# Kernel optimization log

Measured on AMD Instinct MI355X. Metric: run time of the kernel, lower is better.

The kernel has to match this reference:

```python
import jax, jax.numpy as jnp
import numpy as np

NPX = 128      # nPxPup
FOV = 512      # fovInPixel = 2*samp*nPxPup, samp=2
NMODES = 54    # len(jModes)
BATCH = 8
ALPHA = np.pi / 2


def _make_consts():
    # circular pupil on the nPxPup grid
    x = np.linspace(-1.0, 1.0, NPX)
    X, Y = np.meshgrid(x, x)
    pupil = ((X ** 2 + Y ** 2) <= 1.0).astype(np.float32)
    # 4-faced pyramid phase mask on the FOV grid, pre-fftshifted
    f = np.arange(FOV) - FOV / 2
    FX, FY = np.meshgrid(f, f)
    pyr_phase = ALPHA * (np.abs(FX) + np.abs(FY))
    pyr_mask = np.fft.fftshift(np.exp(-1j * pyr_phase)).astype(np.complex64)
    return pupil, pyr_mask


def setup_inputs() -> dict:
    key = jax.random.key(0)
    k1, k2 = jax.random.split(key)
    pupil_np, mask_np = _make_consts()
    pupil = jnp.asarray(pupil_np)                      # [NPX,NPX] float32
    pyrMask = jnp.asarray(mask_np)                     # [FOV,FOV] complex64 (fftshifted)
    # Zernike-like mode basis restricted to the pupil, column-major modes as in the torch buffer
    modes = jax.random.normal(k1, (NPX * NPX, NMODES), dtype=jnp.float32) * pupil.reshape(-1, 1)
    OL1 = (jnp.eye(NMODES, dtype=jnp.float32) * 0.1)   # learnable parameter
    inputs = jax.random.normal(k2, (BATCH, 1, NPX, NPX), dtype=jnp.float32) * pupil
    return {"inputs": inputs, "modes": modes, "OL1": OL1, "pupil": pupil, "pyrMask": pyrMask}


def _prop(phase, pupil, pyrMask):
    """Vanilla pyramid WFS propagation (modulation=0).
    phase: [B,1,NPX,NPX] -> intensity [B,1,FOV,FOV]."""
    u = (pupil * jnp.exp(1j * phase)).astype(jnp.complex64)
    npv = (FOV - NPX) // 2
    field = jnp.zeros(phase.shape[:2] + (FOV, FOV), dtype=jnp.complex64)
    field = field.at[:, :, npv:npv + NPX, npv:npv + NPX].set(u)
    buf = jnp.fft.fft2(field) * pyrMask          # focal plane * pyramid mask
    return jnp.abs(jnp.fft.fft2(buf)) ** 2       # detector intensity


def reference(inputs, modes, OL1, pupil, pyrMask):
    n_modes = OL1.shape[0]
    optModes = modes @ OL1                                     # [NPX*NPX, M]
    # reference (flat wavefront) intensity
    flat = (jnp.ones((NPX, NPX), jnp.float32) * (pupil > 0))[None, None]
    I0 = _prop(flat, pupil, pyrMask)
    I0 = I0 / jnp.sum(I0)                                      # [1,1,FOV,FOV]
    gainRow = jnp.sum(OL1, axis=1)                             # [M]
    # batch the per-mode +/- push-pull propagations in one FFT pass
    zim = optModes.T.reshape(n_modes, 1, NPX, NPX)
    phases = jnp.concatenate([zim, -zim], axis=0)              # [2M,1,NPX,NPX]
    I4 = _prop(phases, pupil, pyrMask)
    I4 = I4 / jnp.sum(I4, axis=(1, 2, 3), keepdims=True)
    sp = I4[:n_modes] - I0
    sm = I4[n_modes:] - I0
    MZc = 0.5 * (sp - sm) / gainRow[:, None, None, None]
    IM = MZc.reshape(n_modes, -1).T                            # [FOV*FOV, M]
    CM = jnp.linalg.pinv(IM)                                   # [M, FOV*FOV]
    # measurement
    Ip = _prop(inputs, pupil, pyrMask)                         # [B,1,FOV,FOV]
    Inorm = jnp.sum(Ip, axis=(1, 2, 3), keepdims=True)
    Ip = Ip / Inorm - I0
    y = CM @ Ip.reshape(Ip.shape[0], -1).T                     # [M, B]
    return y
```

## Files before the change

kernel.cpp:

```cpp
#include <hip/hip_runtime.h>
#include <math.h>

#define NPIXK 262144
#define ROWF2 584
#define ROWF2B 585

__device__ __forceinline__ int padi8(int i) { return i + (i >> 3); }
__device__ __forceinline__ int padi(int i) { return i + (i >> 5); }

#define WSYNC asm volatile("s_waitcnt lgkmcnt(0)" ::: "memory")

__device__ __forceinline__ float2 cmul(float2 a, float2 b) {
    return make_float2(a.x * b.x - a.y * b.y, a.x * b.y + a.y * b.x);
}

__device__ __forceinline__ void twchain(float ang, float2 tw[8]) {
    float s, c;
    sincosf(ang, &s, &c);
    float2 w1 = make_float2(c, s);
    float2 w2 = cmul(w1, w1);
    float2 w4 = cmul(w2, w2);
    tw[1] = w1;
    tw[2] = w2;
    tw[3] = cmul(w1, w2);
    tw[4] = w4;
    tw[5] = cmul(w1, w4);
    tw[6] = cmul(w2, w4);
    tw[7] = cmul(tw[3], w4);
}

__device__ __forceinline__ void fft8f(float vr[8], float vi[8]) {
    float er[4], ei[4], orr[4], oi[4];
    {
        float t0r = vr[0] + vr[4], t0i = vi[0] + vi[4];
        float t1r = vr[0] - vr[4], t1i = vi[0] - vi[4];
        float t2r = vr[2] + vr[6], t2i = vi[2] + vi[6];
        float t3r = vi[2] - vi[6], t3i = vr[6] - vr[2];
        er[0] = t0r + t2r; ei[0] = t0i + t2i;
        er[1] = t1r + t3r; ei[1] = t1i + t3i;
        er[2] = t0r - t2r; ei[2] = t0i - t2i;
        er[3] = t1r - t3r; ei[3] = t1i - t3i;
    }
    {
        float t0r = vr[1] + vr[5], t0i = vi[1] + vi[5];
        float t1r = vr[1] - vr[5], t1i = vi[1] - vi[5];
        float t2r = vr[3] + vr[7], t2i = vi[3] + vi[7];
        float t3r = vi[3] - vi[7], t3i = vr[7] - vr[3];
        orr[0] = t0r + t2r; oi[0] = t0i + t2i;
        orr[1] = t1r + t3r; oi[1] = t1i + t3i;
        orr[2] = t0r - t2r; oi[2] = t0i - t2i;
        orr[3] = t1r - t3r; oi[3] = t1i - t3i;
    }
    const float c = 0.70710678118654752440f;
    vr[0] = er[0] + orr[0]; vi[0] = ei[0] + oi[0];
    vr[4] = er[0] - orr[0]; vi[4] = ei[0] - oi[0];
    float t1r = c * (orr[1] + oi[1]), t1i = c * (oi[1] - orr[1]);
    vr[1] = er[1] + t1r; vi[1] = ei[1] + t1i;
    vr[5] = er[1] - t1r; vi[5] = ei[1] - t1i;
    float t2r = oi[2], t2i = -orr[2];
    vr[2] = er[2] + t2r; vi[2] = ei[2] + t2i;
    vr[6] = er[2] - t2r; vi[6] = ei[2] - t2i;
    float t3r = c * (oi[3] - orr[3]), t3i = -c * (orr[3] + oi[3]);
    vr[3] = er[3] + t3r; vi[3] = ei[3] + t3i;
    vr[7] = er[3] - t3r; vi[7] = ei[3] - t3i;
}

__device__ __forceinline__ void fft8_s34(float vr[8], float vi[8]) {
    const float c = 0.70710678118654752440f;
    float x3r = vr[3], x3i = vi[3], x4r = vr[4], x4i = vi[4];
    float A = c * (x3r + x3i), B = c * (x3r - x3i);
    vr[0] = x3r + x4r; vi[0] = x3i + x4i;
    vr[1] = -B - x4r;  vi[1] = -A - x4i;
    vr[2] = x4r - x3i; vi[2] = x3r + x4i;
    vr[3] = A - x4r;   vi[3] = -B - x4i;
    vr[4] = x4r - x3r; vi[4] = x4i - x3i;
    vr[5] = B - x4r;   vi[5] = A - x4i;
    vr[6] = x3i + x4r; vi[6] = x4i - x3r;
    vr[7] = -A - x4r;  vi[7] = B - x4i;
}

template <int SPARSE>
__device__ __forceinline__ void fft512v(float2* L, int t,
                                        float vr[8], float vi[8]) {
    if (SPARSE) fft8_s34(vr, vi); else fft8f(vr, vi);
    {
        float2* wb = L + 9 * t;
#pragma unroll
        for (int r = 0; r < 8; ++r) wb[r] = make_float2(vr[r], vi[r]);
    }
    float2 tw[8];
    twchain((float)(t & 7) * -0.09817477042468103870f, tw);
    WSYNC;
    {
        const float2* rb = L + t + (t >> 3);
        { float2 a = rb[0]; vr[0] = a.x; vi[0] = a.y; }
#pragma unroll
        for (int r = 1; r < 8; ++r) {
            float2 a = rb[72 * r];
            float2 w = tw[r];
            vr[r] = a.x * w.x - a.y * w.y;
            vi[r] = a.x * w.y + a.y * w.x;
        }
        fft8f(vr, vi);
        WSYNC;
        float2* wb = L + 9 * t;
#pragma unroll
        for (int r = 0; r < 8; ++r) wb[r] = make_float2(vr[r], vi[r]);
    }
    twchain((float)t * -0.01227184630308512985f, tw);
    WSYNC;
    {
        const float2* rb = L + 9 * (t & 7) + (t >> 3);
        { float2 a = rb[0]; vr[0] = a.x; vi[0] = a.y; }
#pragma unroll
        for (int r = 1; r < 8; ++r) {
            float2 a = rb[72 * r];
            float2 w = tw[r];
            vr[r] = a.x * w.x - a.y * w.y;
            vi[r] = a.x * w.y + a.y * w.x;
        }
        fft8f(vr, vi);
    }
}

template <int SPARSE>
__device__ __forceinline__ void fft512v2(float2* LA, float2* LB, int t,
                                         float avr[8], float avi[8],
                                         float bvr[8], float bvi[8]) {
    if (SPARSE) { fft8_s34(avr, avi); fft8_s34(bvr, bvi); }
    else        { fft8f(avr, avi);   fft8f(bvr, bvi); }
    {
        float2* wa = LA + 9 * t;
        float2* wb = LB + 9 * t;
#pragma unroll
        for (int r = 0; r < 8; ++r) wa[r] = make_float2(avr[r], avi[r]);
#pragma unroll
        for (int r = 0; r < 8; ++r) wb[r] = make_float2(bvr[r], bvi[r]);
    }
    float2 tw[8];
    twchain((float)(t & 7) * -0.09817477042468103870f, tw);
    WSYNC;
    {
        const float2* ra = LA + t + (t >> 3);
        const float2* rb = LB + t + (t >> 3);
        { float2 a = ra[0]; avr[0] = a.x; avi[0] = a.y; }
        { float2 b = rb[0]; bvr[0] = b.x; bvi[0] = b.y; }
#pragma unroll
        for (int r = 1; r < 8; ++r) {
            float2 a = ra[72 * r], b = rb[72 * r], w = tw[r];
            avr[r] = a.x * w.x - a.y * w.y;  avi[r] = a.x * w.y + a.y * w.x;
            bvr[r] = b.x * w.x - b.y * w.y;  bvi[r] = b.x * w.y + b.y * w.x;
        }
        fft8f(avr, avi); fft8f(bvr, bvi);
        WSYNC;
        float2* wa = LA + 9 * t;
        float2* wb = LB + 9 * t;
#pragma unroll
        for (int r = 0; r < 8; ++r) wa[r] = make_float2(avr[r], avi[r]);
#pragma unroll
        for (int r = 0; r < 8; ++r) wb[r] = make_float2(bvr[r], bvi[r]);
    }
    twchain((float)t * -0.01227184630308512985f, tw);
    WSYNC;
    {
        const float2* ra = LA + 9 * (t & 7) + (t >> 3);
        const float2* rb = LB + 9 * (t & 7) + (t >> 3);
        { float2 a = ra[0]; avr[0] = a.x; avi[0] = a.y; }
        { float2 b = rb[0]; bvr[0] = b.x; bvi[0] = b.y; }
#pragma unroll
        for (int r = 1; r < 8; ++r) {
            float2 a = ra[72 * r], b = rb[72 * r], w = tw[r];
            avr[r] = a.x * w.x - a.y * w.y;  avi[r] = a.x * w.y + a.y * w.x;
            bvr[r] = b.x * w.x - b.y * w.y;  bvi[r] = b.x * w.y + b.y * w.x;
        }
        fft8f(avr, avi); fft8f(bvr, bvi);
    }
}

#define FFT_LDS __shared__ float2 lds[4][ROWF2];

__device__ __forceinline__ double lsx(int i) {
    if (i == 127) return 1.0;
    return __dadd_rn(__dmul_rn((double)i, 2.0 / 127.0), -1.0);
}
__device__ __forceinline__ double pupilAt(int r, int c) {
    double xc = lsx(c), xr = lsx(r);
    double s = __dadd_rn(__dmul_rn(xc, xc), __dmul_rn(xr, xr));
    return (s <= 1.0) ? 1.0 : 0.0;
}

__global__ __launch_bounds__(256, 8) void k_s1(const float* __restrict__ optT,
                                               const float* __restrict__ inputs,
                                               float2* __restrict__ T1, int giBase) {
    FFT_LDS
    int tid = threadIdx.x, w = tid >> 6, t = tid & 63;
    int r = (blockIdx.x & 31) * 4 + w;
    int im = blockIdx.x >> 5;
    int gi;
    if (giBase >= 0)            gi = giBase + im;
    else if (giBase == -1)      gi = (im == 0) ? 0 : 108 + im;
    else                        gi = (im < 9) ? ((im == 0) ? 0 : 108 + im)
                                              : im - 8;

    float vr[8], vi[8];
#pragma unroll
    for (int q = 0; q < 8; ++q) { vr[q] = 0.f; vi[q] = 0.f; }
#pragma unroll
    for (int h = 0; h < 2; ++h) {
        int c = t + 64 * h;
        int p = r * 128 + c;
        float pu = (float)pupilAt(r, c);
        float ph;
        if (gi == 0) {
            ph = pu;
        } else if (gi < 109) {
            ph = optT[(gi - 1) * 16384 + p];
        } else {
            ph = inputs[(gi - 109) * 16384 + p];
        }
        float s, cs; sincosf(ph, &s, &cs);
        vr[3 + h] = pu * cs; vi[3 + h] = pu * s;
    }
    fft512v<1>(lds[w], t, vr, vi);
    WSYNC;
#pragma unroll
    for (int q = 0; q < 8; ++q) {
        int d = t + 64 * q;
        lds[w][padi8(d)] = make_float2(vr[q], vi[q]);
    }
    __syncthreads();
    int r0 = (blockIdx.x & 31) * 4;
    float2* dst = T1 + (size_t)im * 65536;
#pragma unroll
    for (int it = 0; it < 8; ++it) {
        int g = it * 256 + tid;
        int l = g >> 2, rr = g & 3;
        dst[(size_t)l * 128 + r0 + rr] = lds[rr][padi8(l)];
    }
}

__global__ __launch_bounds__(256, 4) void k_s23(const float2* __restrict__ T1,
                                                float2* __restrict__ C2p) {
    __shared__ float2 lds[8][ROWF2B];
    int tid = threadIdx.x, w = tid >> 6, t = tid & 63;
    int imgL = blockIdx.x >> 6;
    int l0 = (blockIdx.x & 63) * 8;
    int lA = l0 + w, lB = l0 + 4 + w;
    const float2* srcA = T1 + (size_t)imgL * 65536 + (size_t)lA * 128;
    const float2* srcB = T1 + (size_t)imgL * 65536 + (size_t)lB * 128;
    float avr[8], avi[8], bvr[8], bvi[8];
#pragma unroll
    for (int q = 0; q < 8; ++q) { avr[q] = 0.f; avi[q] = 0.f; bvr[q] = 0.f; bvi[q] = 0.f; }
    { float2 a0 = srcA[t], a1 = srcA[t + 64];
      avr[3] = a0.x; avi[3] = a0.y; avr[4] = a1.x; avi[4] = a1.y; }
    { float2 b0 = srcB[t], b1 = srcB[t + 64];
      bvr[3] = b0.x; bvi[3] = b0.y; bvr[4] = b1.x; bvi[4] = b1.y; }
    fft512v2<1>(lds[w], lds[w + 4], t, avr, avi, bvr, bvi);
    int glA = (lA <= 256) ? lA : 512 - lA;
    int glB = (lB <= 256) ? lB : 512 - lB;
#pragma unroll
    for (int q = 0; q < 8; ++q) {
        int k = t + 64 * q;
        int gk = (k <= 256) ? k : 512 - k;
        {   int n = (gk + glA) & 3;
            float a = avr[q], b = avi[q], X, Y;
            if (n == 0)      { X = a;  Y = b;  }
            else if (n == 1) { X = b;  Y = -a; }
            else if (n == 2) { X = -a; Y = -b; }
            else             { X = -b; Y = a;  }
            avr[q] = X; avi[q] = Y; }
        {   int n = (gk + glB) & 3;
            float a = bvr[q], b = bvi[q], X, Y;
            if (n == 0)      { X = a;  Y = b;  }
            else if (n == 1) { X = b;  Y = -a; }
            else if (n == 2) { X = -a; Y = -b; }
            else             { X = -b; Y = a;  }
            bvr[q] = X; bvi[q] = Y; }
    }
    fft512v2<0>(lds[w], lds[w + 4], t, avr, avi, bvr, bvi);
    WSYNC;
#pragma unroll
    for (int q = 0; q < 8; ++q) {
        int d = padi8(t + 64 * q);
        lds[w][d]     = make_float2(avr[q], avi[q]);
        lds[w + 4][d] = make_float2(bvr[q], bvi[q]);
    }
    __syncthreads();
    float2* dst = C2p + (size_t)imgL * NPIXK;
#pragma unroll
    for (int it = 0; it < 16; ++it) {
        int g = it * 256 + tid;
        int p = g >> 3, rr = g & 7;
        dst[(size_t)p * 512 + l0 + rr] = lds[rr][padi8(p)];
    }
}

__global__ __launch_bounds__(256, 8) void k_s4(const float2* __restrict__ C2,
                                               float* __restrict__ dst,
                                               const float* __restrict__ I0,
                                               int ep) {
    FFT_LDS
    int tid = threadIdx.x, w = tid >> 6, t = tid & 63;
    int imgL = blockIdx.x >> 7, p = (blockIdx.x & 127) * 4 + w;
    const float2* src = C2 + (size_t)imgL * NPIXK + (size_t)p * 512;
    float vr[8], vi[8];
#pragma unroll
    for (int q = 0; q < 8; ++q) { float2 a = src[t + 64 * q]; vr[q] = a.x; vi[q] = a.y; }
    fft512v<0>(lds[w], t, vr, vi);
    size_t rowOff = (size_t)p * 512;
    float* drow = dst + (size_t)imgL * NPIXK + rowOff;
    if (ep == 0) {
#pragma unroll
        for (int q = 0; q < 8; ++q) {
            int k = t + 64 * q;
            drow[k] = vr[q] * vr[q] + vi[q] * vi[q];
        }
    } else {
#pragma unroll
        for (int q = 0; q < 8; ++q) {
            int k = t + 64 * q;
            float mag2 = vr[q] * vr[q] + vi[q] * vi[q];
            drow[k] = mag2 - I0[rowOff + k];
        }
    }
}

__global__ __launch_bounds__(256, 8) void k_s4pm(const float2* __restrict__ C2p,
                                                 float* __restrict__ dst,
                                                 const double* __restrict__ gainInv,
                                                 int gBase) {
    FFT_LDS
    int tid = threadIdx.x, w = tid >> 6, t = tid & 63;
    int imgL = blockIdx.x >> 7, q2 = blockIdx.x & 127;
    int p = 2 * q2 + (w & 1) + (w >> 1) * 256;
    const float2* src = C2p + (size_t)imgL * NPIXK + (size_t)p * 512;
    float vr[8], vi[8], m2[8];
#pragma unroll
    for (int q = 0; q < 8; ++q) { float2 a = src[t + 64 * q]; vr[q] = a.x; vi[q] = a.y; }
    fft512v<0>(lds[w], t, vr, vi);
    WSYNC;
    float* mrow = (float*)lds[w];
#pragma unroll
    for (int q = 0; q < 8; ++q) {
        m2[q] = vr[q] * vr[q] + vi[q] * vi[q];
        mrow[padi(t + 64 * q)] = m2[q];
    }
    __syncthreads();
    float g = (float)gainInv[gBase + imgL];
    float* drow = dst + (size_t)imgL * NPIXK + (size_t)p * 512;
    const float* prow = (const float*)lds[w ^ 2];
#pragma unroll
    for (int q = 0; q < 8; ++q) {
        int qp = (q + 4) & 7;
        float other = prow[padi(t + 64 * qp)];
        drow[t + 64 * q] = g * (m2[q] - other);
    }
}

__global__ __launch_bounds__(256, 8) void k_s4x(const float2* __restrict__ C2p,
                                                float* __restrict__ I0buf,
                                                float* __restrict__ Mz,
                                                const double* __restrict__ gainInv) {
    FFT_LDS
    int tid = threadIdx.x, w = tid >> 6, t = tid & 63;
    int im = blockIdx.x >> 7, b7 = blockIdx.x & 127;
    if (im < 9) {
        int p = b7 * 4 + w;
        const float2* src = C2p + (size_t)im * NPIXK + (size_t)p * 512;
        float vr[8], vi[8];
#pragma unroll
        for (int q = 0; q < 8; ++q) { float2 a = src[t + 64 * q]; vr[q] = a.x; vi[q] = a.y; }
        fft512v<0>(lds[w], t, vr, vi);
        float* drow = I0buf + (size_t)im * NPIXK + (size_t)p * 512;
#pragma unroll
        for (int q = 0; q < 8; ++q) {
            int k = t + 64 * q;
            drow[k] = vr[q] * vr[q] + vi[q] * vi[q];
        }
    } else {
        int mi = im - 9;
        int p = 2 * b7 + (w & 1) + (w >> 1) * 256;
        const float2* src = C2p + (size_t)im * NPIXK + (size_t)p * 512;
        float vr[8], vi[8], m2[8];
#pragma unroll
        for (int q = 0; q < 8; ++q) { float2 a = src[t + 64 * q]; vr[q] = a.x; vi[q] = a.y; }
        fft512v<0>(lds[w], t, vr, vi);
        WSYNC;
        float* mrow = (float*)lds[w];
#pragma unroll
        for (int q = 0; q < 8; ++q) {
            m2[q] = vr[q] * vr[q] + vi[q] * vi[q];
            mrow[padi(t + 64 * q)] = m2[q];
        }
        __syncthreads();
        float g = (float)gainInv[mi];
        float* drow = Mz + (size_t)mi * NPIXK + (size_t)p * 512;
        const float* prow = (const float*)lds[w ^ 2];
#pragma unroll
        for (int q = 0; q < 8; ++q) {
            int qp = (q + 4) & 7;
            float other = prow[padi(t + 64 * qp)];
            drow[t + 64 * q] = g * (m2[q] - other);
        }
    }
}

__global__ __launch_bounds__(256) void k_modes(const float* __restrict__ modes,
                                               const float* __restrict__ OL1,
                                               float* __restrict__ optT,
                                               double* __restrict__ gainInv,
                                               double* __restrict__ G,
                                               double* __restrict__ bmat) {
    __shared__ float sM[64 * 54];
    __shared__ float sOL[54 * 54];
    int tid = threadIdx.x;
    if (blockIdx.x == 0) {
        for (int i = tid; i < 54 * 54; i += 256) G[i] = 0.0;
        for (int i = tid; i < 54 * 8; i += 256) bmat[i] = 0.0;
    }
    for (int i = tid; i < 54 * 54; i += 256) sOL[i] = OL1[i];
    const float* msrc = modes + (size_t)blockIdx.x * 64 * 54;
    for (int i = tid; i < 64 * 54; i += 256) sM[i] = msrc[i];
    __syncthreads();
    int pl = tid & 63, mg = tid >> 6;
    int p = blockIdx.x * 64 + pl;
    const float* mrow = sM + pl * 54;
    for (int m = mg; m < 54; m += 4) {
        double acc = 0.0;
#pragma unroll
        for (int j = 0; j < 54; ++j)
            acc += (double)mrow[j] * (double)sOL[j * 54 + m];
        optT[(size_t)m * 16384 + p] = (float)acc;
    }
    if (blockIdx.x == 0 && tid < 54) {
        double g = 0.0;
        for (int j = 0; j < 54; ++j) g += (double)sOL[tid * 54 + j];
        gainInv[tid] = 0.5 / g;
    }
}

__device__ __forceinline__ float dot4(float4 a, float4 b) {
    return a.x * b.x + a.y * b.y + a.z * b.z + a.w * b.w;
}

#define GPROWS 2304
__global__ __launch_bounds__(256, 4) void k_gram54(const float* __restrict__ Mz,
                                                   const float* __restrict__ V,
                                                   const float* __restrict__ I0,
                                                   float* __restrict__ part,
                                                   int subI0) {
    __shared__ float Ms[64 * 128];
    int tid = threadIdx.x;
    int task = tid / 7, sl = tid - task * 7;
    if (task > 35) task = 35;
    int oi = 0, rem = task;
    while (rem >= 8 - oi) { rem -= 8 - oi; ++oi; }
    int oj = oi + rem;
    int ra = 8 * oi, rb = 8 * oj;
    int start = (32 * sl) / 7, len = (32 * (sl + 1)) / 7 - start;
    int rot = tid % len;
    float s[64];
#pragma unroll
    for (int q = 0; q < 64; ++q) s[q] = 0.f;

#pragma unroll 1
    for (int ch = 0; ch < 2; ++ch) {
        size_t P0 = ((size_t)blockIdx.x * 2 + ch) * 128;
        if (ch) __syncthreads();
        for (int idx = tid; idx < 64 * 32; idx += 256) {
            int i = idx >> 5, v4 = idx & 31;
            float4 vv;
            if (i < 54) {
                vv = *(const float4*)(Mz + (size_t)i * NPIXK + P0 + v4 * 4);
            } else if (i < 62) {
                vv = *(const float4*)(V + (size_t)(i - 54) * NPIXK + P0 + v4 * 4);
                if (subI0) {
                    float4 i0 = *(const float4*)(I0 + P0 + v4 * 4);
                    vv.x -= i0.x; vv.y -= i0.y; vv.z -= i0.z; vv.w -= i0.w;
                }
            } else {
                vv = make_float4(0.f, 0.f, 0.f, 0.f);
            }
            ((float4*)Ms)[i * 32 + (v4 ^ (i >> 3))] = vv;
        }
        __syncthreads();
#pragma unroll 1
        for (int k = 0; k < 5; ++k) {
            if (k < len) {
                int kk = k + rot; if (kk >= len) kk -= len;
                int pp = start + kk;
                int colA = pp ^ oi, colB = pp ^ oj;
                float4 b[8];
#pragma unroll
                for (int j = 0; j < 8; ++j)
                    b[j] = ((const float4*)Ms)[(rb + j) * 32 + colB];
#pragma unroll
                for (int i = 0; i < 8; ++i) {
                    float4 a = ((const float4*)Ms)[(ra + i) * 32 + colA];
#pragma unroll
                    for (int j = 0; j < 8; ++j) {
                        float acc = s[i * 8 + j];
                        acc = fmaf(a.x, b[j].x, acc);
                        acc = fmaf(a.y, b[j].y, acc);
                        acc = fmaf(a.z, b[j].z, acc);
                        acc = fmaf(a.w, b[j].w, acc);
                        s[i * 8 + j] = acc;
                    }
                }
            }
        }
    }
    float* red = Ms;
    float* dst = part + (size_t)blockIdx.x * GPROWS;
#pragma unroll
    for (int c = 0; c < 4; ++c) {
        __syncthreads();
        if (tid < 252) {
#pragma unroll
            for (int q = 0; q < 4; ++q)
                ((float4*)(red + tid * 16))[q] =
                    make_float4(s[c * 16 + 4 * q], s[c * 16 + 4 * q + 1],
                                s[c * 16 + 4 * q + 2], s[c * 16 + 4 * q + 3]);
        }
        __syncthreads();
        for (int idx = tid; idx < 576; idx += 256) {
            int tk = idx >> 4, j = idx & 15;
            float acc = 0.f;
#pragma unroll
            for (int ss = 0; ss < 7; ++ss) acc += red[(tk * 7 + ss) * 16 + j];
            dst[tk * 64 + c * 16 + j] = acc;
        }
    }
}

__global__ __launch_bounds__(256) void k_gred54(const float* __restrict__ part,
                                                double* __restrict__ G,
                                                double* __restrict__ bmat) {
    __shared__ double red[8][33];
    int tid = threadIdx.x;
    int r = tid & 31, grp = tid >> 5;
    int row = blockIdx.x * 32 + r;
    int bid0 = blockIdx.y * 256;
    double acc = 0.0;
    for (int k = 0; k < 32; ++k)
        acc += (double)part[(size_t)(bid0 + grp + 8 * k) * GPROWS + row];
    red[grp][r] = acc;
    __syncthreads();
    if (tid < 32) {
        int rr = blockIdx.x * 32 + tid;
        double s = 0.0;
#pragma unroll
        for (int g = 0; g < 8; ++g) s += red[g][tid];
        int tk = rr >> 6, q = rr & 63;
        int oi = 0, rem = tk;
        while (rem >= 8 - oi) { rem -= 8 - oi; ++oi; }
        int oj = oi + rem;
        int a = 8 * oi + (q >> 3), b = 8 * oj + (q & 7);
        if (a < 54) {
            if (b < 54) {
                if (a <= b) atomicAdd(&G[a * 54 + b], s);
            } else if (b < 62) {
                atomicAdd(&bmat[a * 8 + (b - 54)], s);
            }
        }
    }
}

__global__ __launch_bounds__(256) void k_gram(const float* __restrict__ Mz,
                                              const float* __restrict__ V,
                                              const float* __restrict__ I0,
                                              float* __restrict__ part,
                                              int cA, int PROWS, int subI0) {
    __shared__ float Ms[54 * 128];
    __shared__ float Vs[8 * 128];
    int tid = threadIdx.x;
    int cQ = (cA + 3) >> 2;
    int nQT = cQ * (cQ + 1) / 2;
    int nT = nQT + cQ * 8;
    int task = tid;
    int kind = (task < nQT) ? 0 : (task < nT ? 1 : 2);
    int r0[4], r1[4], bb = 0, Ti = 0, Tj = 0, Qi = 0;
    if (kind == 0) {
        int rem = task;
        while (rem >= cQ - Ti) { rem -= cQ - Ti; ++Ti; }
        Tj = Ti + rem;
#pragma unroll
        for (int q = 0; q < 4; ++q) {
            int i = 4 * Ti + q; r0[q] = (i < cA) ? i : cA - 1;
            int j = 4 * Tj + q; r1[q] = (j < cA) ? j : cA - 1;
        }
    } else if (kind == 1) {
        int tb = task - nQT;
        Qi = tb >> 3; bb = tb & 7;
#pragma unroll
        for (int q = 0; q < 4; ++q) {
            int i = 4 * Qi + q; r0[q] = (i < cA) ? i : cA - 1;
        }
    }
    float s[16];
#pragma unroll
    for (int q = 0; q < 16; ++q) s[q] = 0.f;

    size_t P0 = (size_t)blockIdx.x * 128;
    for (int idx = tid; idx < cA * 32; idx += 256) {
        int i = idx >> 5, v4 = idx & 31;
        ((float4*)Ms)[i * 32 + v4] =
            *(const float4*)(Mz + (size_t)i * NPIXK + P0 + v4 * 4);
    }
    for (int idx = tid; idx < 8 * 32; idx += 256) {
        int b = idx >> 5, v4 = idx & 31;
        float4 vv = *(const float4*)(V + (size_t)b * NPIXK + P0 + v4 * 4);
        if (subI0) {
            float4 i0 = *(const float4*)(I0 + P0 + v4 * 4);
            vv.x -= i0.x; vv.y -= i0.y; vv.z -= i0.z; vv.w -= i0.w;
        }
        ((float4*)Vs)[b * 32 + v4] = vv;
    }
    __syncthreads();
    if (kind == 0) {
        for (int kk = 0; kk < 32; ++kk) {
            int pp = (kk + tid) & 31;
            float4 a0 = ((float4*)(Ms + r0[0] * 128))[pp];
            float4 a1 = ((float4*)(Ms + r0[1] * 128))[pp];
            float4 a2 = ((float4*)(Ms + r0[2] * 128))[pp];
            float4 a3 = ((float4*)(Ms + r0[3] * 128))[pp];
            float4 b0 = ((float4*)(Ms + r1[0] * 128))[pp];
            float4 b1 = ((float4*)(Ms + r1[1] * 128))[pp];
            float4 b2 = ((float4*)(Ms + r1[2] * 128))[pp];
            float4 b3 = ((float4*)(Ms + r1[3] * 128))[pp];
            s[0] += dot4(a0, b0); s[1] += dot4(a0, b1);
            s[2] += dot4(a0, b2); s[3] += dot4(a0, b3);
            s[4] += dot4(a1, b0); s[5] += dot4(a1, b1);
            s[6] += dot4(a1, b2); s[7] += dot4(a1, b3);
            s[8] += dot4(a2, b0); s[9] += dot4(a2, b1);
            s[10] += dot4(a2, b2); s[11] += dot4(a2, b3);
            s[12] += dot4(a3, b0); s[13] += dot4(a3, b1);
            s[14] += dot4(a3, b2); s[15] += dot4(a3, b3);
        }
    } else if (kind == 1) {
        for (int kk = 0; kk < 32; ++kk) {
            int pp = (kk + tid) & 31;
            float4 vb = ((float4*)Vs)[bb * 32 + pp];
            float4 a0 = ((float4*)(Ms + r0[0] * 128))[pp];
            float4 a1 = ((float4*)(Ms + r0[1] * 128))[pp];
            float4 a2 = ((float4*)(Ms + r0[2] * 128))[pp];
            float4 a3 = ((float4*)(Ms + r0[3] * 128))[pp];
            s[0] += dot4(a0, vb); s[1] += dot4(a1, vb);
            s[2] += dot4(a2, vb); s[3] += dot4(a3, vb);
        }
    }
    float* dst = part + (size_t)blockIdx.x * PROWS;
    if (kind == 0) {
#pragma unroll
        for (int q = 0; q < 16; ++q) dst[task * 16 + q] = s[q];
    } else if (kind == 1) {
#pragma unroll
        for (int q = 0; q < 4; ++q)
            dst[nQT * 16 + (task - nQT) * 4 + q] = s[q];
    }
}

__global__ __launch_bounds__(256) void k_gred3(const float* __restrict__ part,
                                               double* __restrict__ G,
                                               double* __restrict__ bmat,
                                               int cA, int m0, int PROWS) {
    __shared__ double red[8][33];
    int tid = threadIdx.x;
    int r = tid & 31, grp = tid >> 5;
    int row = blockIdx.x * 32 + r;
    int bid0 = blockIdx.y * 256;
    double acc = 0.0;
    if (row < PROWS)
        for (int k = 0; k < 32; ++k)
            acc += (double)part[(size_t)(bid0 + grp + 8 * k) * PROWS + row];
    red[grp][r] = acc;
    __syncthreads();
    if (tid < 32) {
        int rr = blockIdx.x * 32 + tid;
        if (rr < PROWS) {
            double s = 0.0;
#pragma unroll
            for (int g = 0; g < 8; ++g) s += red[g][tid];
            int cQ = (cA + 3) >> 2;
            int nQT = cQ * (cQ + 1) / 2;
            if (rr < nQT * 16) {
                int tile = rr >> 4, q = rr & 15;
                int Ti = 0, rem = tile;
                while (rem >= cQ - Ti) { rem -= cQ - Ti; ++Ti; }
                int Tj = Ti + rem;
                int i = 4 * Ti + (q >> 2), j = 4 * Tj + (q & 3);
                if (i < cA && j < cA && i <= j)
                    atomicAdd(&G[(m0 + i) * 54 + (m0 + j)], s);
            } else {
                int qb = rr - nQT * 16;
                int tb = qb >> 2, qq = qb & 3;
                int Qi = tb >> 3, bbb = tb & 7;
                int i = 4 * Qi + qq;
                if (i < cA) atomicAdd(&bmat[(m0 + i) * 8 + bbb], s);
            }
        }
    }
}

__global__ __launch_bounds__(256) void k_gramx(const float* __restrict__ MzA,
                                               const float* __restrict__ MzB,
                                               double* __restrict__ G,
                                               int cA, int m0, int mb) {
    __shared__ float Ms[54 * 128];
    __shared__ float Bs[128];
    int tid = threadIdx.x;
    double acc = 0.0;
    for (int ch = 0; ch < 4; ++ch) {
        size_t P0 = (size_t)blockIdx.x * 512 + (size_t)ch * 128;
        __syncthreads();
        for (int idx = tid; idx < cA * 32; idx += 256) {
            int i = idx >> 5, v4 = idx & 31;
            ((float4*)Ms)[i * 32 + v4] =
                *(const float4*)(MzA + (size_t)i * NPIXK + P0 + v4 * 4);
        }
        if (tid < 128) Bs[tid] = MzB[P0 + tid];
        __syncthreads();
        if (tid < cA) {
            const float* ri = Ms + tid * 128;
            float s = 0.f;
            for (int k = 0; k < 128; ++k) {
                int p = (k + tid) & 127;
                s += ri[p] * Bs[p];
            }
            acc += (double)s;
        }
    }
    if (tid < cA) atomicAdd(&G[(m0 + tid) * 54 + mb], acc);
}

__global__ __launch_bounds__(512) void k_solve(const double* __restrict__ G,
                                               const double* __restrict__ bmat,
                                               float* __restrict__ out) {
    __shared__ double A[54][65];
    int tid = threadIdx.x;
    int r = tid >> 3, cg = tid & 7;
    for (int idx = tid; idx < 54 * 62; idx += 512) {
        int i = idx / 62, c = idx % 62;
        A[i][c] = (c < 54) ? ((i <= c) ? G[i * 54 + c] : G[c * 54 + i])
                           : bmat[i * 8 + (c - 54)];
    }
    __syncthreads();
    for (int p = 0; p < 54; ++p) {
        double f = 0.0;
        bool act = (r < 54) && (r != p);
        if (act) f = A[r][p] / A[p][p];
        __syncthreads();
        if (act) {
#pragma unroll
            for (int k = 0; k < 8; ++k) {
                int c = cg + 8 * k;
                if (c < 62) A[r][c] -= f * A[p][c];
            }
        }
        __syncthreads();
    }
    for (int idx = tid; idx < 54 * 8; idx += 512) {
        int m = idx >> 3, b = idx & 7;
        out[idx] = (float)(A[m][54 + b] / A[m][m]);
    }
}

__global__ void k_zero(float* out, int n) {
    int i = blockIdx.x * 256 + threadIdx.x;
    if (i < n) out[i] = 0.f;
}

extern "C" void kernel_launch(void* const* d_in, const int* in_sizes, int n_in,
                              void* d_out, int out_size, void* d_ws, size_t ws_size,
                              hipStream_t stream) {
    float* out = (float*)d_out;
    if (out_size <= 0) return;
    if (n_in < 3 || in_sizes[0] != 131072 || in_sizes[1] != 884736 ||
        in_sizes[2] != 2916 || out_size < 432) {
        k_zero<<<(out_size + 255) / 256, 256, 0, stream>>>(out, out_size);
        return;
    }
    const float* inputs = (const float*)d_in[0];
    const float* modes  = (const float*)d_in[1];
    const float* OL1    = (const float*)d_in[2];

    char* ws = (char*)d_ws;
    size_t off = 0;
    auto alloc = [&](size_t bytes) -> void* {
        void* p = ws + off;
        off += (bytes + 255) & ~(size_t)255;
        return p;
    };
    float*  optT    = (float*)  alloc((size_t)54 * 16384 * 4);
    double* gainInv = (double*) alloc(64 * 8);
    double* G       = (double*) alloc(54 * 54 * 8);
    double* bmat    = (double*) alloc(54 * 8 * 8);
    float*  I0buf   = (float*)  alloc((size_t)9 * NPIXK * 4);
    float*  V       = I0buf + NPIXK;
    float*  MzB1    = (float*)  alloc((size_t)NPIXK * 4);
    float*  part    = (float*)  alloc((size_t)2048 * GPROWS * 4);

    const size_t IMG  = (size_t)NPIXK * 4 + 256;
    const size_t PIPE = ((size_t)65536 * 8 + 256) + ((size_t)NPIXK * 8 + 256);
    size_t rem = (ws_size > off + 4096) ? ws_size - off - 4096 : 0;
    int cA, chunkP;
    if (rem >= 54 * IMG + PIPE) {
        cA = 54;
        size_t c = (rem - 54 * IMG) / PIPE;
        chunkP = (c > 63) ? 63 : (int)c;
        if (chunkP < 1) chunkP = 1;
    } else if (rem >= IMG + PIPE) {
        cA = (int)((rem - PIPE) / IMG);
        if (cA > 53) cA = 53;
        if (cA < 1) cA = 1;
        size_t left = rem - (size_t)cA * IMG;
        chunkP = (int)(left / PIPE);
        if (chunkP < 1) chunkP = 1;
        if (chunkP > cA) chunkP = cA;
    } else {
        k_zero<<<(out_size + 255) / 256, 256, 0, stream>>>(out, out_size);
        return;
    }
    float*  MzA = (float*)  alloc((size_t)cA * NPIXK * 4);
    float2* T1  = (float2*) alloc((size_t)chunkP * 65536 * 8);
    float2* C2p = (float2*) alloc((size_t)chunkP * NPIXK * 8);
    if (off > ws_size) {
        k_zero<<<(out_size + 255) / 256, 256, 0, stream>>>(out, out_size);
        return;
    }

    auto prop_one = [&](int giBase, int n, float* dst, int ep) {
        for (int s = 0; s < n; s += chunkP) {
            int nn = n - s; if (nn > chunkP) nn = chunkP;
            k_s1<<<nn * 32, 256, 0, stream>>>(optT, inputs, T1, giBase + s);
            k_s23<<<nn * 64, 256, 0, stream>>>(T1, C2p);
            k_s4<<<nn * 128, 256, 0, stream>>>(C2p, dst + (size_t)s * NPIXK,
                                               I0buf, ep);
        }
    };
    auto prop_pm = [&](int m0, int n, float* dst, int gBase) {
        for (int s = 0; s < n; s += chunkP) {
            int nn = n - s; if (nn > chunkP) nn = chunkP;
            k_s1<<<nn * 32, 256, 0, stream>>>(optT, inputs, T1, 1 + m0 + s);
            k_s23<<<nn * 64, 256, 0, stream>>>(T1, C2p);
            k_s4pm<<<nn * 128, 256, 0, stream>>>(C2p,
                                                 dst + (size_t)s * NPIXK,
                                                 gainInv, gBase + s);
        }
    };

    k_modes<<<256, 256, 0, stream>>>(modes, OL1, optT, gainInv, G, bmat);

    if (cA >= 54 && chunkP >= 63) {
        k_s1<<<63 * 32, 256, 0, stream>>>(optT, inputs, T1, -2);
        k_s23<<<63 * 64, 256, 0, stream>>>(T1, C2p);
        k_s4x<<<63 * 128, 256, 0, stream>>>(C2p, I0buf, MzA, gainInv);
        k_gram54<<<1024, 256, 0, stream>>>(MzA, V, I0buf, part, 1);
        k_gred54<<<dim3(72, 4), 256, 0, stream>>>(part, G, bmat);
    } else {
        int subI0;
        if (chunkP >= 9) {
            k_s1<<<9 * 32, 256, 0, stream>>>(optT, inputs, T1, -1);
            k_s23<<<9 * 64, 256, 0, stream>>>(T1, C2p);
            k_s4<<<9 * 128, 256, 0, stream>>>(C2p, I0buf, I0buf, 0);
            subI0 = 1;
        } else {
            prop_one(0, 1, I0buf, 0);
            prop_one(109, 8, V, 2);
            subI0 = 0;
        }
        if (cA >= 54) {
            prop_pm(0, 54, MzA, 0);
            k_gram54<<<1024, 256, 0, stream>>>(MzA, V, I0buf, part, subI0);
            k_gred54<<<dim3(72, 4), 256, 0, stream>>>(part, G, bmat);
        } else {
            for (int m0 = 0; m0 < 54; m0 += cA) {
                int ca = 54 - m0; if (ca > cA) ca = cA;
                prop_pm(m0, ca, MzA, m0);
                int cQ = (ca + 3) >> 2;
                int PROWS = cQ * (cQ + 1) / 2 * 16 + cQ * 32;
                k_gram<<<2048, 256, 0, stream>>>(MzA, V, I0buf, part, ca, PROWS,
                                                 subI0);
                k_gred3<<<dim3((PROWS + 31) / 32, 8), 256, 0, stream>>>(part, G,
                                                                       bmat, ca,
                                                                       m0, PROWS);
                for (int mb = m0 + ca; mb < 54; ++mb) {
                    prop_pm(mb, 1, MzB1, mb);
                    k_gramx<<<512, 256, 0, stream>>>(MzA, MzB1, G, ca, m0, mb);
                }
            }
        }
    }
    k_solve<<<1, 512, 0, stream>>>(G, bmat, out);
}
```

Measured before the change: 247.4 us.

## Pair mirrored rows per wave in k_s4x and drop redundant solve barrier

k_s4x now has each wave run two 512-point row FFTs together via fft512v2. In the push/pull branch the mirrored rows p and p+256 are handled by the same wave, so the difference is formed in registers instead of through an LDS exchange and a block barrier. The grid is halved and launch bounds are relaxed to 4 blocks per CU, trading occupancy for more work per wave. In k_solve, one __syncthreads per pivot step is removed. This relies on the eight threads of each row sitting in the same wave64, with a compiler fence keeping the read of the pivot factor ahead of the writes.

New measurement: 242.5 us. About the same (-2.0%).

```diff
diff --git a/kernel.cpp b/kernel.cpp
--- a/kernel.cpp
+++ b/kernel.cpp
@@ -9,6 +9,7 @@
 __device__ __forceinline__ int padi(int i) { return i + (i >> 5); }
 
 #define WSYNC asm volatile("s_waitcnt lgkmcnt(0)" ::: "memory")
+#define CFENCE asm volatile("" ::: "memory")
 
 __device__ __forceinline__ float2 cmul(float2 a, float2 b) {
     return make_float2(a.x * b.x - a.y * b.y, a.x * b.y + a.y * b.x);
@@ -357,50 +358,59 @@
     }
 }
 
-__global__ __launch_bounds__(256, 8) void k_s4x(const float2* __restrict__ C2p,
+__global__ __launch_bounds__(256, 4) void k_s4x(const float2* __restrict__ C2p,
                                                 float* __restrict__ I0buf,
                                                 float* __restrict__ Mz,
                                                 const double* __restrict__ gainInv) {
-    FFT_LDS
+    __shared__ float2 lds[8][ROWF2B];
     int tid = threadIdx.x, w = tid >> 6, t = tid & 63;
-    int im = blockIdx.x >> 7, b7 = blockIdx.x & 127;
+    int im = blockIdx.x >> 6, b6 = blockIdx.x & 63;
+    float avr[8], avi[8], bvr[8], bvi[8];
     if (im < 9) {
-        int p = b7 * 4 + w;
-        const float2* src = C2p + (size_t)im * NPIXK + (size_t)p * 512;
-        float vr[8], vi[8];
-#pragma unroll
-        for (int q = 0; q < 8; ++q) { float2 a = src[t + 64 * q]; vr[q] = a.x; vi[q] = a.y; }
-        fft512v<0>(lds[w], t, vr, vi);
-        float* drow = I0buf + (size_t)im * NPIXK + (size_t)p * 512;
+        int pA = b6 * 8 + w, pB = b6 * 8 + 4 + w;
+        const float2* srcA = C2p + (size_t)im * NPIXK + (size_t)pA * 512;
+        const float2* srcB = C2p + (size_t)im * NPIXK + (size_t)pB * 512;
+#pragma unroll
+        for (int q = 0; q < 8; ++q) {
+            float2 a = srcA[t + 64 * q]; avr[q] = a.x; avi[q] = a.y;
+            float2 b = srcB[t + 64 * q]; bvr[q] = b.x; bvi[q] = b.y;
+        }
+        fft512v2<0>(lds[w], lds[w + 4], t, avr, avi, bvr, bvi);
+        float* dA = I0buf + (size_t)im * NPIXK + (size_t)pA * 512;
+        float* dB = I0buf + (size_t)im * NPIXK + (size_t)pB * 512;
 #pragma unroll
         for (int q = 0; q < 8; ++q) {
             int k = t + 64 * q;
-            drow[k] = vr[q] * vr[q] + vi[q] * vi[q];
+            dA[k] = avr[q] * avr[q] + avi[q] * avi[q];
+            dB[k] = bvr[q] * bvr[q] + bvi[q] * bvi[q];
         }
     } else {
         int mi = im - 9;
-        int p = 2 * b7 + (w & 1) + (w >> 1) * 256;
-        const float2* src = C2p + (size_t)im * NPIXK + (size_t)p * 512;
-        float vr[8], vi[8], m2[8];
-#pragma unroll
-        for (int q = 0; q < 8; ++q) { float2 a = src[t + 64 * q]; vr[q] = a.x; vi[q] = a.y; }
-        fft512v<0>(lds[w], t, vr, vi);
-        WSYNC;
-        float* mrow = (float*)lds[w];
+        int pA = b6 * 4 + w;
+        int pB = pA + 256;
+        const float2* srcA = C2p + (size_t)im * NPIXK + (size_t)pA * 512;
+        const float2* srcB = C2p + (size_t)im * NPIXK + (size_t)pB * 512;
 #pragma unroll
         for (int q = 0; q < 8; ++q) {
-            m2[q] = vr[q] * vr[q] + vi[q] * vi[q];
-            mrow[padi(t + 64 * q)] = m2[q];
-        }
-        __syncthreads();
+            float2 a = srcA[t + 64 * q]; avr[q] = a.x; avi[q] = a.y;
+            float2 b = srcB[t + 64 * q]; bvr[q] = b.x; bvi[q] = b.y;
+        }
+        fft512v2<0>(lds[w], lds[w + 4], t, avr, avi, bvr, bvi);
+        float m2A[8], m2B[8];
+#pragma unroll
+        for (int q = 0; q < 8; ++q) {
+            m2A[q] = avr[q] * avr[q] + avi[q] * avi[q];
+            m2B[q] = bvr[q] * bvr[q] + bvi[q] * bvi[q];
+        }
         float g = (float)gainInv[mi];
-        float* drow = Mz + (size_t)mi * NPIXK + (size_t)p * 512;
-        const float* prow = (const float*)lds[w ^ 2];
+        float* dA = Mz + (size_t)mi * NPIXK + (size_t)pA * 512;
+        float* dB = Mz + (size_t)mi * NPIXK + (size_t)pB * 512;
 #pragma unroll
         for (int q = 0; q < 8; ++q) {
+            int k = t + 64 * q;
             int qp = (q + 4) & 7;
-            float other = prow[padi(t + 64 * qp)];
-            drow[t + 64 * q] = g * (m2[q] - other);
+            dA[k] = g * (m2A[q] - m2B[qp]);
+            dB[k] = g * (m2B[q] - m2A[qp]);
         }
     }
 }
@@ -746,11 +756,10 @@
     }
     __syncthreads();
     for (int p = 0; p < 54; ++p) {
-        double f = 0.0;
         bool act = (r < 54) && (r != p);
-        if (act) f = A[r][p] / A[p][p];
-        __syncthreads();
         if (act) {
+            double f = A[r][p] / A[p][p];
+            CFENCE;
 #pragma unroll
             for (int k = 0; k < 8; ++k) {
                 int c = cg + 8 * k;
@@ -854,7 +863,7 @@
     if (cA >= 54 && chunkP >= 63) {
         k_s1<<<63 * 32, 256, 0, stream>>>(optT, inputs, T1, -2);
         k_s23<<<63 * 64, 256, 0, stream>>>(T1, C2p);
-        k_s4x<<<63 * 128, 256, 0, stream>>>(C2p, I0buf, MzA, gainInv);
+        k_s4x<<<63 * 64, 256, 0, stream>>>(C2p, I0buf, MzA, gainInv);
         k_gram54<<<1024, 256, 0, stream>>>(MzA, V, I0buf, part, 1);
         k_gred54<<<dim3(72, 4), 256, 0, stream>>>(part, G, bmat);
     } else {
```
